# Kernel optimization log

Measured on AMD Instinct MI355X. Metric: run time of the kernel, lower is better.

The kernel has to match this reference:

```python
import jax, jax.numpy as jnp
import numpy as np

B, T, H = 4096, 200, 64
NU, NI, NC = 100000, 1000000, 1000
AU_HID = 36
EPS = 1e-8


def dice(x, alpha):
    # Dice activation: p = sigmoid(batchnorm(x)); out = p*x + (1-p)*alpha*x
    axes = tuple(range(x.ndim - 1))
    m = jnp.mean(x, axis=axes, keepdims=True)
    v = jnp.var(x, axis=axes, keepdims=True)
    p = jax.nn.sigmoid((x - m) * jax.lax.rsqrt(v + EPS))
    return p * x + (1.0 - p) * alpha * x


def setup_inputs() -> dict:
    key = jax.random.key(0)
    ks = jax.random.split(key, 18)
    s = 0.02
    n = lambda k, shp: (jax.random.normal(k, shp, dtype=jnp.float32) * s)
    return {
        "user": jax.random.randint(ks[0], (B,), 0, NU),
        "hist": jax.random.randint(ks[1], (B, T), 0, NI),
        "item": jax.random.randint(ks[2], (B,), 0, NI),
        "cate": jax.random.randint(ks[3], (B,), 0, NC),
        "U": n(ks[4], (NU, H)),
        "I": n(ks[5], (NI, H)),
        "C": n(ks[6], (NC, H)),
        "au_W1": n(ks[7], (4 * H, AU_HID)),
        "au_b1": jnp.zeros((AU_HID,), jnp.float32),
        "au_a1": jnp.zeros((AU_HID,), jnp.float32),
        "au_W2": n(ks[8], (AU_HID, 1)),
        "au_b2": jnp.zeros((1,), jnp.float32),
        "W1": n(ks[9], (4 * H, 80)),
        "b1": jnp.zeros((80,), jnp.float32),
        "a1": jnp.zeros((80,), jnp.float32),
        "W2": n(ks[10], (80, 40)),
        "b2": jnp.zeros((40,), jnp.float32),
        "a2": jnp.zeros((40,), jnp.float32),
        "W3": n(ks[11], (40, 2)),
        "b3": jnp.zeros((2,), jnp.float32),
    }


def reference(user, hist, item, cate, U, I, C,
              au_W1, au_b1, au_a1, au_W2, au_b2,
              W1, b1, a1, W2, b2, a2, W3, b3):
    ue = U[user]            # [B,H]
    ie = I[item]            # [B,H]
    ce = C[cate]            # [B,H]
    he = I[hist]            # [B,T,H] history item embeddings (vectorized over the time loop)
    ieb = jnp.broadcast_to(ie[:, None, :], he.shape)
    # ActivationUnit: concat(hist, item, hist-item, hist*item) -> Linear -> Dice -> Linear(->1)
    au_in = jnp.concatenate([he, ieb, he - ieb, he * ieb], axis=-1)  # [B,T,4H]
    h1 = dice(au_in @ au_W1 + au_b1, au_a1)                          # [B,T,36]
    w = h1 @ au_W2 + au_b2                                           # [B,T,1]
    # weighted-sum pooling over history (original detaches via numpy round-trip)
    cur = jax.lax.stop_gradient(jnp.sum(w * he, axis=1))             # [B,H]
    x = jnp.concatenate([ue, ie, ce, cur], axis=-1)                  # [B,4H]
    x = dice(x @ W1 + b1, a1)
    x = dice(x @ W2 + b2, a2)
    return x @ W3 + b3                                               # [B,2]
```

## Files before the change

kernel.cpp:

```cpp
#include <hip/hip_runtime.h>
#include <math.h>

#define BB 4096
#define TT 200
#define NT (BB*TT)

typedef __attribute__((ext_vector_type(8))) __bf16 bf16x8;
typedef __attribute__((ext_vector_type(4))) float f32x4;
typedef __attribute__((ext_vector_type(2))) _Float16 f16x2;

static __device__ __forceinline__ unsigned short f2b(float f) {
  __bf16 b = (__bf16)f;
  return __builtin_bit_cast(unsigned short, b);
}

__global__ __launch_bounds__(256) void k_prep_we(const float* __restrict__ auW1,
                                                 float* __restrict__ WE) {
  int i = blockIdx.x * 256 + threadIdx.x;
  if (i < 64 * 36) WE[i] = auW1[i] + auW1[128 * 36 + i];
}

__global__ __launch_bounds__(64) void k_prep_tb(const int* __restrict__ item,
                                                const float* __restrict__ Itab,
                                                const float* __restrict__ auW1,
                                                const float* __restrict__ auB1,
                                                float* __restrict__ TBuf) {
  int b = blockIdx.x, tid = threadIdx.x;
  __shared__ float sIe[64];
  sIe[tid] = Itab[(size_t)item[b] * 64 + tid];
  __syncthreads();
  if (tid < 36) {
    float a = auB1[tid];
    for (int k = 0; k < 64; ++k)
      a += sIe[k] * (auW1[(64 + k) * 36 + tid] - auW1[(128 + k) * 36 + tid]);
    TBuf[b * 36 + tid] = a;
  }
}

__global__ __launch_bounds__(256) void k_prep_w1t(const float* __restrict__ W1,
                                                  float* __restrict__ W1T) {
  int j = blockIdx.x, k = threadIdx.x;
  W1T[j * 256 + k] = W1[k * 80 + j];
}

__global__ __launch_bounds__(256, 4) void k_gemm1(
    const int* __restrict__ hist, const int* __restrict__ item,
    const float* __restrict__ Itab, const float* __restrict__ WE,
    const float* __restrict__ WD, const float* __restrict__ TBuf,
    float* __restrict__ PART, _Float16* __restrict__ Xb) {
  const int b = blockIdx.x, tid = threadIdx.x;
  const int wv = tid >> 6, l = tid & 63;
  const int lr = l & 15, lq = l >> 4;
  __shared__ __align__(16) unsigned short sWBT[48 * 72];
  __shared__ float sIe[64];
  __shared__ float sR1[192], sR2[192];

  if (tid < 64) sIe[tid] = Itab[(size_t)item[b] * 64 + tid];
  __syncthreads();
  for (int i = tid; i < 64 * 48; i += 256) {
    int k = i / 48, n = i - (i / 48) * 48;
    float w = 0.f;
    if (n < 36) { int idx = k * 36 + n; w = WE[idx] + sIe[k] * WD[idx]; }
    sWBT[n * 72 + k] = f2b(w);
  }
  __syncthreads();

  bf16x8 bfr[3][2];
#pragma unroll
  for (int nt = 0; nt < 3; ++nt)
#pragma unroll
    for (int kh = 0; kh < 2; ++kh)
      bfr[nt][kh] = *reinterpret_cast<const bf16x8*>(
          sWBT + (nt * 16 + lr) * 72 + kh * 32 + lq * 8);

  float tb3[3];
#pragma unroll
  for (int nt = 0; nt < 3; ++nt) {
    int j = nt * 16 + lr;
    tb3[nt] = (j < 36) ? TBuf[b * 36 + j] : 0.f;
  }

  const int* hp = hist + b * TT;
  f32x4 acc[4][3];
#pragma unroll
  for (int mi = 0; mi < 4; ++mi)
#pragma unroll
    for (int nt = 0; nt < 3; ++nt) acc[mi][nt] = (f32x4){0.f, 0.f, 0.f, 0.f};

#pragma unroll
  for (int mi = 0; mi < 4; ++mi) {
    const int mt = wv + mi * 4;
    if (mt <= 12) {
      int trow = mt * 16 + lr;
      int row = hp[trow < TT ? trow : (TT - 1)];
      const float* rp = Itab + (size_t)row * 64;
      const float4* rp4 = (const float4*)(rp + lq * 8);
      float4 v0 = rp4[0];
      float4 v1 = rp4[1];
      const float4* rp4b = (const float4*)(rp + 32 + lq * 8);
      float4 v2 = rp4b[0];
      float4 v3 = rp4b[1];
      bf16x8 a0, a1;
      a0[0] = (__bf16)v0.x; a0[1] = (__bf16)v0.y; a0[2] = (__bf16)v0.z; a0[3] = (__bf16)v0.w;
      a0[4] = (__bf16)v1.x; a0[5] = (__bf16)v1.y; a0[6] = (__bf16)v1.z; a0[7] = (__bf16)v1.w;
      a1[0] = (__bf16)v2.x; a1[1] = (__bf16)v2.y; a1[2] = (__bf16)v2.z; a1[3] = (__bf16)v2.w;
      a1[4] = (__bf16)v3.x; a1[5] = (__bf16)v3.y; a1[6] = (__bf16)v3.z; a1[7] = (__bf16)v3.w;
#pragma unroll
      for (int nt = 0; nt < 3; ++nt) {
        acc[mi][nt] = __builtin_amdgcn_mfma_f32_16x16x32_bf16(
            a0, bfr[nt][0], acc[mi][nt], 0, 0, 0);
        acc[mi][nt] = __builtin_amdgcn_mfma_f32_16x16x32_bf16(
            a1, bfr[nt][1], acc[mi][nt], 0, 0, 0);
      }
    }
  }

  float s1[3] = {0.f, 0.f, 0.f}, s2[3] = {0.f, 0.f, 0.f};
  _Float16* xrow = Xb + (size_t)b * 7200;
#pragma unroll
  for (int mi = 0; mi < 4; ++mi) {
    const int mt = wv + mi * 4;
    if (mt <= 12) {
#pragma unroll
      for (int q = 0; q < 4; ++q) {
        const int t = mt * 16 + lq * 4 + q;
        if (t < TT) {
#pragma unroll
          for (int nt = 0; nt < 3; ++nt) {
            const int j = nt * 16 + lr;
            float x = acc[mi][nt][q] + tb3[nt];
            if (j < 36) {
              s1[nt] += x;
              s2[nt] = fmaf(x, x, s2[nt]);
              xrow[t * 36 + j] = (_Float16)x;
            }
          }
        }
      }
    }
  }
#pragma unroll
  for (int nt = 0; nt < 3; ++nt) {
    float a = s1[nt], c = s2[nt];
    a += __shfl_xor(a, 16, 64); a += __shfl_xor(a, 32, 64);
    c += __shfl_xor(c, 16, 64); c += __shfl_xor(c, 32, 64);
    if (l < 16) {
      sR1[wv * 48 + nt * 16 + l] = a;
      sR2[wv * 48 + nt * 16 + l] = c;
    }
  }
  __syncthreads();
  if (tid < 36) {
    float a = sR1[tid] + sR1[48 + tid] + sR1[96 + tid] + sR1[144 + tid];
    float c = sR2[tid] + sR2[48 + tid] + sR2[96 + tid] + sR2[144 + tid];
    PART[b * 72 + tid] = a;
    PART[b * 72 + 36 + tid] = c;
  }
}

__global__ __launch_bounds__(256) void k_aust(const float* __restrict__ PART,
                                              float* __restrict__ AUST) {
  int ch = blockIdx.x, tid = threadIdx.x;
  float s1 = 0.f, s2 = 0.f;
  for (int b = tid; b < BB; b += 256) {
    s1 += PART[b * 72 + ch];
    s2 += PART[b * 72 + 36 + ch];
  }
  __shared__ float r1[256], r2[256];
  r1[tid] = s1;
  r2[tid] = s2;
  __syncthreads();
  for (int off = 128; off > 0; off >>= 1) {
    if (tid < off) { r1[tid] += r1[tid + off]; r2[tid] += r2[tid + off]; }
    __syncthreads();
  }
  if (tid == 0) {
    float m = r1[0] / (float)NT;
    float var = r2[0] / (float)NT - m * m;
    AUST[ch] = m;
    AUST[36 + ch] = 1.0f / sqrtf(var + 1e-8f);
  }
}

__global__ __launch_bounds__(256) void k_att(
    const int* __restrict__ hist, const int* __restrict__ user,
    const int* __restrict__ item, const int* __restrict__ cate,
    const float* __restrict__ Itab, const float* __restrict__ Utab,
    const float* __restrict__ Ctab, const _Float16* __restrict__ Xb,
    const float* __restrict__ AUST, const float* __restrict__ auA1,
    const float* __restrict__ auW2, const float* __restrict__ auB2,
    const float* __restrict__ W1T, const float* __restrict__ b1,
    float* __restrict__ Y1) {
  const int b = blockIdx.x, tid = threadIdx.x;
  __shared__ float sW[TT];
  __shared__ int sRows[TT];
  __shared__ float sD[144];
  __shared__ float sPart[256];
  __shared__ float sX[256];
  if (tid < TT) sRows[tid] = hist[b * TT + tid];
  if (tid >= 208 && tid < 208 + 36) sD[tid - 208] = AUST[tid - 208];
  else if (tid < 36) sD[36 + tid] = AUST[36 + tid];
  else if (tid >= 64 && tid < 100) sD[72 + (tid - 64)] = auA1[tid - 64];
  else if (tid >= 128 && tid < 164) sD[108 + (tid - 128)] = auW2[tid - 128];
  __syncthreads();
  if (tid < TT) {
    const f16x2* xr = (const f16x2*)(Xb + (size_t)b * 7200 + tid * 36);
    float w = auB2[0];
#pragma unroll
    for (int p = 0; p < 18; ++p) {
      f16x2 pr = xr[p];
#pragma unroll
      for (int h = 0; h < 2; ++h) {
        int j = 2 * p + h;
        float x = (float)pr[h];
        float xh = (x - sD[j]) * sD[36 + j];
        float pp = 1.0f / (1.0f + __expf(-xh));
        float al = sD[72 + j];
        w = fmaf(x * (al + pp * (1.0f - al)), sD[108 + j], w);
      }
    }
    sW[tid] = w;
  }
  __syncthreads();
  {
    const int l = tid & 63, wv = tid >> 6;
    float c = 0.f;
    const int t0 = wv * 50;
#pragma unroll 5
    for (int u = t0; u < t0 + 50; ++u) {
      int r = sRows[u];
      c = fmaf(sW[u], Itab[(size_t)r * 64 + l], c);
    }
    sPart[tid] = c;
  }
  __syncthreads();
  if (tid < 64) {
    float cur = sPart[tid] + sPart[64 + tid] + sPart[128 + tid] + sPart[192 + tid];
    sX[tid] = Utab[(size_t)user[b] * 64 + tid];
    sX[64 + tid] = Itab[(size_t)item[b] * 64 + tid];
    sX[128 + tid] = Ctab[(size_t)cate[b] * 64 + tid];
    sX[192 + tid] = cur;
  }
  __syncthreads();
  if (tid < 80) {
    float a = b1[tid];
    const float4* wt = (const float4*)(W1T + tid * 256);
#pragma unroll 8
    for (int kq = 0; kq < 64; ++kq) {
      float4 w4 = wt[kq];
      a = fmaf(sX[kq * 4 + 0], w4.x, a);
      a = fmaf(sX[kq * 4 + 1], w4.y, a);
      a = fmaf(sX[kq * 4 + 2], w4.z, a);
      a = fmaf(sX[kq * 4 + 3], w4.w, a);
    }
    Y1[b * 80 + tid] = a;
  }
}

__global__ __launch_bounds__(256) void k_colstats(const float* __restrict__ src,
                                                  int nch, float* __restrict__ st) {
  int ch = blockIdx.x, tid = threadIdx.x;
  float s1 = 0.f, s2 = 0.f;
  for (int r = tid; r < BB; r += 256) {
    float v = src[r * nch + ch];
    s1 += v;
    s2 += v * v;
  }
  __shared__ float r1[256], r2[256];
  r1[tid] = s1;
  r2[tid] = s2;
  __syncthreads();
  for (int off = 128; off > 0; off >>= 1) {
    if (tid < off) { r1[tid] += r1[tid + off]; r2[tid] += r2[tid + off]; }
    __syncthreads();
  }
  if (tid == 0) {
    float m = r1[0] / (float)BB;
    float var = r2[0] / (float)BB - m * m;
    st[ch] = m;
    st[nch + ch] = 1.0f / sqrtf(var + 1e-8f);
  }
}

__global__ __launch_bounds__(128) void k_mlp2(const float* __restrict__ Y1,
                                              const float* __restrict__ ST80,
                                              const float* __restrict__ a1,
                                              const float* __restrict__ W2,
                                              const float* __restrict__ b2,
                                              float* __restrict__ Y2) {
  int b = blockIdx.x, tid = threadIdx.x;
  __shared__ float sY[80];
  if (tid < 80) {
    float x = Y1[b * 80 + tid];
    float xh = (x - ST80[tid]) * ST80[80 + tid];
    float p = 1.0f / (1.0f + expf(-xh));
    sY[tid] = p * x + (1.0f - p) * a1[tid] * x;
  }
  __syncthreads();
  if (tid < 40) {
    float a = b2[tid];
    for (int k = 0; k < 80; ++k) a += sY[k] * W2[k * 40 + tid];
    Y2[b * 40 + tid] = a;
  }
}

__global__ __launch_bounds__(64) void k_mlp3(const float* __restrict__ Y2,
                                             const float* __restrict__ ST40,
                                             const float* __restrict__ a2,
                                             const float* __restrict__ W3,
                                             const float* __restrict__ b3,
                                             float* __restrict__ out) {
  int b = blockIdx.x, tid = threadIdx.x;
  __shared__ float sY[40];
  if (tid < 40) {
    float x = Y2[b * 40 + tid];
    float xh = (x - ST40[tid]) * ST40[40 + tid];
    float p = 1.0f / (1.0f + expf(-xh));
    sY[tid] = p * x + (1.0f - p) * a2[tid] * x;
  }
  __syncthreads();
  if (tid < 2) {
    float a = b3[tid];
    for (int k = 0; k < 40; ++k) a += sY[k] * W3[k * 2 + tid];
    out[b * 2 + tid] = a;
  }
}

extern "C" void kernel_launch(void* const* d_in, const int* in_sizes, int n_in,
                              void* d_out, int out_size, void* d_ws, size_t ws_size,
                              hipStream_t stream) {
  const int* user = (const int*)d_in[0];
  const int* hist = (const int*)d_in[1];
  const int* item = (const int*)d_in[2];
  const int* cate = (const int*)d_in[3];
  const float* Utab = (const float*)d_in[4];
  const float* Itab = (const float*)d_in[5];
  const float* Ctab = (const float*)d_in[6];
  const float* auW1 = (const float*)d_in[7];
  const float* auB1 = (const float*)d_in[8];
  const float* auA1 = (const float*)d_in[9];
  const float* auW2 = (const float*)d_in[10];
  const float* auB2 = (const float*)d_in[11];
  const float* W1 = (const float*)d_in[12];
  const float* b1 = (const float*)d_in[13];
  const float* a1 = (const float*)d_in[14];
  const float* W2 = (const float*)d_in[15];
  const float* b2 = (const float*)d_in[16];
  const float* a2 = (const float*)d_in[17];
  const float* W3 = (const float*)d_in[18];
  const float* b3 = (const float*)d_in[19];
  float* out = (float*)d_out;

  float* ws = (float*)d_ws;
  float* WE = ws;
  float* TBuf = WE + 2304;
  float* PART = TBuf + BB * 36;
  float* AUST = PART + BB * 72;
  float* Y1 = AUST + 72;
  float* ST80 = Y1 + BB * 80;
  float* Y2 = ST80 + 160;
  float* ST40 = Y2 + BB * 40;
  float* W1T = ST40 + 80;
  _Float16* Xb = (_Float16*)(W1T + 80 * 256);

  const float* WD = auW1 + 192 * 36;

  k_prep_we<<<9, 256, 0, stream>>>(auW1, WE);
  k_prep_tb<<<BB, 64, 0, stream>>>(item, Itab, auW1, auB1, TBuf);
  k_prep_w1t<<<80, 256, 0, stream>>>(W1, W1T);
  k_gemm1<<<BB, 256, 0, stream>>>(hist, item, Itab, WE, WD, TBuf, PART, Xb);
  k_aust<<<36, 256, 0, stream>>>(PART, AUST);
  k_att<<<BB, 256, 0, stream>>>(hist, user, item, cate, Itab, Utab, Ctab, Xb,
                                AUST, auA1, auW2, auB2, W1T, b1, Y1);
  k_colstats<<<80, 256, 0, stream>>>(Y1, 80, ST80);
  k_mlp2<<<BB, 128, 0, stream>>>(Y1, ST80, a1, W2, b2, Y2);
  k_colstats<<<40, 256, 0, stream>>>(Y2, 40, ST40);
  k_mlp3<<<BB, 64, 0, stream>>>(Y2, ST40, a2, W3, b3, out);
}
```

Before: 201.1 us.

## Fold prep kernels into gemm1 and stage history rows in LDS

Removes three preprocessing launches: the folded weight matrix and the per-batch item bias are now computed inside k_gemm1, and the W1 transpose runs in extra blocks of k_aust. k_gemm1 also gathers all 200 history rows into shared memory as bf16 with coalesced float4 loads before the MFMA loop, instead of each lane fetching scattered rows directly. This cuts launch overhead and intermediate buffers but adds about 29KB of LDS per block, which may lower occupancy, and repeats the bias computation in every block.

New measurement: 252.3 us. 1.25x slower.

```diff
diff --git a/kernel.cpp b/kernel.cpp
--- a/kernel.cpp
+++ b/kernel.cpp
@@ -14,55 +14,58 @@
   return __builtin_bit_cast(unsigned short, b);
 }
 
-__global__ __launch_bounds__(256) void k_prep_we(const float* __restrict__ auW1,
-                                                 float* __restrict__ WE) {
-  int i = blockIdx.x * 256 + threadIdx.x;
-  if (i < 64 * 36) WE[i] = auW1[i] + auW1[128 * 36 + i];
-}
-
-__global__ __launch_bounds__(64) void k_prep_tb(const int* __restrict__ item,
-                                                const float* __restrict__ Itab,
-                                                const float* __restrict__ auW1,
-                                                const float* __restrict__ auB1,
-                                                float* __restrict__ TBuf) {
-  int b = blockIdx.x, tid = threadIdx.x;
-  __shared__ float sIe[64];
-  sIe[tid] = Itab[(size_t)item[b] * 64 + tid];
-  __syncthreads();
-  if (tid < 36) {
-    float a = auB1[tid];
-    for (int k = 0; k < 64; ++k)
-      a += sIe[k] * (auW1[(64 + k) * 36 + tid] - auW1[(128 + k) * 36 + tid]);
-    TBuf[b * 36 + tid] = a;
-  }
-}
-
-__global__ __launch_bounds__(256) void k_prep_w1t(const float* __restrict__ W1,
-                                                  float* __restrict__ W1T) {
-  int j = blockIdx.x, k = threadIdx.x;
-  W1T[j * 256 + k] = W1[k * 80 + j];
-}
-
 __global__ __launch_bounds__(256, 4) void k_gemm1(
     const int* __restrict__ hist, const int* __restrict__ item,
-    const float* __restrict__ Itab, const float* __restrict__ WE,
-    const float* __restrict__ WD, const float* __restrict__ TBuf,
-    float* __restrict__ PART, _Float16* __restrict__ Xb) {
+    const float* __restrict__ Itab, const float* __restrict__ auW1,
+    const float* __restrict__ auB1, float* __restrict__ PART,
+    _Float16* __restrict__ Xb) {
   const int b = blockIdx.x, tid = threadIdx.x;
   const int wv = tid >> 6, l = tid & 63;
   const int lr = l & 15, lq = l >> 4;
+  __shared__ __align__(16) unsigned short sHe[200 * 72];
   __shared__ __align__(16) unsigned short sWBT[48 * 72];
-  __shared__ float sIe[64];
   __shared__ float sR1[192], sR2[192];
 
-  if (tid < 64) sIe[tid] = Itab[(size_t)item[b] * 64 + tid];
-  __syncthreads();
+  const float ie_reg = Itab[(size_t)item[b] * 64 + l];
+
+  const int* hp = hist + b * TT;
+  for (int i = tid; i < 200 * 16; i += 256) {
+    int r = i >> 4, q = i & 15;
+    const float4 v = ((const float4*)(Itab + (size_t)hp[r] * 64))[q];
+    ushort4 u;
+    u.x = f2b(v.x); u.y = f2b(v.y); u.z = f2b(v.z); u.w = f2b(v.w);
+    *(ushort4*)(sHe + r * 72 + q * 4) = u;
+  }
+
+  const float* Wc = auW1 + 128 * 36;
+  const float* Wd = auW1 + 192 * 36;
   for (int i = tid; i < 64 * 48; i += 256) {
     int k = i / 48, n = i - (i / 48) * 48;
     float w = 0.f;
-    if (n < 36) { int idx = k * 36 + n; w = WE[idx] + sIe[k] * WD[idx]; }
+    if (n < 36) {
+      int idx = k * 36 + n;
+      float iek = __shfl(ie_reg, k, 64);
+      w = (auW1[idx] + Wc[idx]) + iek * Wd[idx];
+    }
     sWBT[n * 72 + k] = f2b(w);
   }
+
+  const float* Wb_ = auW1 + 64 * 36;
+  float tb3[3];
+#pragma unroll
+  for (int nt = 0; nt < 3; ++nt) {
+    int j = nt * 16 + lr;
+    tb3[nt] = (j < 36) ? auB1[j] : 0.f;
+  }
+  for (int k = 0; k < 64; ++k) {
+    float iek = __shfl(ie_reg, k, 64);
+#pragma unroll
+    for (int nt = 0; nt < 3; ++nt) {
+      int j = nt * 16 + lr;
+      if (j < 36) tb3[nt] = fmaf(iek, Wb_[k * 36 + j] - Wc[k * 36 + j], tb3[nt]);
+    }
+  }
+
   __syncthreads();
 
   bf16x8 bfr[3][2];
@@ -73,14 +76,6 @@
       bfr[nt][kh] = *reinterpret_cast<const bf16x8*>(
           sWBT + (nt * 16 + lr) * 72 + kh * 32 + lq * 8);
 
-  float tb3[3];
-#pragma unroll
-  for (int nt = 0; nt < 3; ++nt) {
-    int j = nt * 16 + lr;
-    tb3[nt] = (j < 36) ? TBuf[b * 36 + j] : 0.f;
-  }
-
-  const int* hp = hist + b * TT;
   f32x4 acc[4][3];
 #pragma unroll
   for (int mi = 0; mi < 4; ++mi)
@@ -91,20 +86,11 @@
   for (int mi = 0; mi < 4; ++mi) {
     const int mt = wv + mi * 4;
     if (mt <= 12) {
-      int trow = mt * 16 + lr;
-      int row = hp[trow < TT ? trow : (TT - 1)];
-      const float* rp = Itab + (size_t)row * 64;
-      const float4* rp4 = (const float4*)(rp + lq * 8);
-      float4 v0 = rp4[0];
-      float4 v1 = rp4[1];
-      const float4* rp4b = (const float4*)(rp + 32 + lq * 8);
-      float4 v2 = rp4b[0];
-      float4 v3 = rp4b[1];
-      bf16x8 a0, a1;
-      a0[0] = (__bf16)v0.x; a0[1] = (__bf16)v0.y; a0[2] = (__bf16)v0.z; a0[3] = (__bf16)v0.w;
-      a0[4] = (__bf16)v1.x; a0[5] = (__bf16)v1.y; a0[6] = (__bf16)v1.z; a0[7] = (__bf16)v1.w;
-      a1[0] = (__bf16)v2.x; a1[1] = (__bf16)v2.y; a1[2] = (__bf16)v2.z; a1[3] = (__bf16)v2.w;
-      a1[4] = (__bf16)v3.x; a1[5] = (__bf16)v3.y; a1[6] = (__bf16)v3.z; a1[7] = (__bf16)v3.w;
+      const int trow0 = mt * 16 + lr;
+      const int trow = trow0 < TT ? trow0 : (TT - 1);
+      const unsigned short* ap = sHe + trow * 72 + lq * 8;
+      bf16x8 a0 = *reinterpret_cast<const bf16x8*>(ap);
+      bf16x8 a1 = *reinterpret_cast<const bf16x8*>(ap + 32);
 #pragma unroll
       for (int nt = 0; nt < 3; ++nt) {
         acc[mi][nt] = __builtin_amdgcn_mfma_f32_16x16x32_bf16(
@@ -159,8 +145,16 @@
 }
 
 __global__ __launch_bounds__(256) void k_aust(const float* __restrict__ PART,
-                                              float* __restrict__ AUST) {
-  int ch = blockIdx.x, tid = threadIdx.x;
+                                              const float* __restrict__ W1,
+                                              float* __restrict__ AUST,
+                                              float* __restrict__ W1T) {
+  int blk = blockIdx.x, tid = threadIdx.x;
+  if (blk >= 36) {
+    int j = blk - 36;
+    W1T[j * 256 + tid] = W1[tid * 80 + j];
+    return;
+  }
+  int ch = blk;
   float s1 = 0.f, s2 = 0.f;
   for (int b = tid; b < BB; b += 256) {
     s1 += PART[b * 72 + ch];
@@ -352,9 +346,7 @@
   float* out = (float*)d_out;
 
   float* ws = (float*)d_ws;
-  float* WE = ws;
-  float* TBuf = WE + 2304;
-  float* PART = TBuf + BB * 36;
+  float* PART = ws;
   float* AUST = PART + BB * 72;
   float* Y1 = AUST + 72;
   float* ST80 = Y1 + BB * 80;
@@ -363,13 +355,8 @@
   float* W1T = ST40 + 80;
   _Float16* Xb = (_Float16*)(W1T + 80 * 256);
 
-  const float* WD = auW1 + 192 * 36;
-
-  k_prep_we<<<9, 256, 0, stream>>>(auW1, WE);
-  k_prep_tb<<<BB, 64, 0, stream>>>(item, Itab, auW1, auB1, TBuf);
-  k_prep_w1t<<<80, 256, 0, stream>>>(W1, W1T);
-  k_gemm1<<<BB, 256, 0, stream>>>(hist, item, Itab, WE, WD, TBuf, PART, Xb);
-  k_aust<<<36, 256, 0, stream>>>(PART, AUST);
+  k_gemm1<<<BB, 256, 0, stream>>>(hist, item, Itab, auW1, auB1, PART, Xb);
+  k_aust<<<116, 256, 0, stream>>>(PART, W1, AUST, W1T);
   k_att<<<BB, 256, 0, stream>>>(hist, user, item, cate, Itab, Utab, Ctab, Xb,
                                 AUST, auA1, auW2, auB2, W1T, b1, Y1);
   k_colstats<<<80, 256, 0, stream>>>(Y1, 80, ST80);
```
